# Kernel tuning notes

Hardware: AMD Instinct MI355X
Metric: run time of the kernel (lower is better)

The kernel has to match this reference:

```python
import jax, jax.numpy as jnp
import numpy as np
import math

B, T, C, E, H = 16, 256, 6, 512, 8


def setup_inputs() -> dict:
    key = jax.random.key(0)
    ks = jax.random.split(key, 5)
    std = 0.02
    return {
        "x": jax.random.normal(ks[0], (B, T, C, E), dtype=jnp.float32),
        "Wq": jax.random.normal(ks[1], (E, E), dtype=jnp.float32) * std,
        "bq": jnp.zeros((E,), dtype=jnp.float32),
        "Wk": jax.random.normal(ks[2], (E, E), dtype=jnp.float32) * std,
        "bk": jnp.zeros((E,), dtype=jnp.float32),
        "Wv": jax.random.normal(ks[3], (E, E), dtype=jnp.float32) * std,
        "bv": jnp.zeros((E,), dtype=jnp.float32),
        "Wp": jax.random.normal(ks[4], (E, E), dtype=jnp.float32) * std,
        "bp": jnp.zeros((E,), dtype=jnp.float32),
    }


def reference(x, Wq, bq, Wk, bk, Wv, bv, Wp, bp):
    b, t, c, e = x.shape
    hd = e // H
    # nn.Linear: y = x @ W^T + b, then view(B,T,C,H,hd).transpose(1,3) -> (B,H,C,T,hd)
    def heads(W, bias):
        y = jnp.einsum('btce,fe->btcf', x, W) + bias
        return y.reshape(b, t, c, H, hd).transpose(0, 3, 2, 1, 4)  # B,H,C,T,hd

    q = heads(Wq, bq)
    k = heads(Wk, bk)
    v = heads(Wv, bv)

    scale = 1.0 / math.sqrt(hd)
    att = jnp.einsum('bhctd,bhcsd->bhcts', q, k) * scale  # B,H,C,T,T
    causal = jnp.tril(jnp.ones((t, t), dtype=bool))
    att = jnp.where(causal, att, -jnp.inf)
    att = jax.nn.softmax(att, axis=-1)

    y = jnp.einsum('bhcts,bhcsd->bhctd', att, v)  # B,H,C,T,hd
    # permute(0,3,1,2,4) -> (B,T,H,C,hd), then view(B,T,C,E) (faithful to torch)
    y = y.transpose(0, 3, 1, 2, 4).reshape(b, t, c, e)
    return jnp.einsum('btce,fe->btcf', y, Wp) + bp
```

## Files before the change

### kernel.cpp

```cpp
#include <hip/hip_runtime.h>


typedef unsigned short u16;
typedef short bf16x8 __attribute__((ext_vector_type(8)));
typedef float f32x4 __attribute__((ext_vector_type(4)));
typedef u16 u16x4 __attribute__((ext_vector_type(4)));

#define MFMA16(a, b, c) __builtin_amdgcn_mfma_f32_16x16x32_bf16((a), (b), (c), 0, 0, 0)

__device__ __forceinline__ u16 f2b(float f) {
  union { float f; unsigned u; } v; v.f = f;
  unsigned r = v.u + 0x7fffu + ((v.u >> 16) & 1u);
  return (u16)(r >> 16);
}
__device__ __forceinline__ void gl_lds16(const void* g, void* l) {
  __builtin_amdgcn_global_load_lds(
      (const __attribute__((address_space(1))) void*)g,
      (__attribute__((address_space(3))) void*)l, 16, 0, 0);
}

__global__ void cvt_w(const float* W0, const float* W1, const float* W2,
                      const float* W3, u16* dst) {
  const float* src = (blockIdx.y == 0) ? W0 : (blockIdx.y == 1) ? W1
                   : (blockIdx.y == 2) ? W2 : W3;
  const int idx = (blockIdx.x * 256 + threadIdx.x) * 4;
  f32x4 v = *(const f32x4*)(src + idx);
  u16x4 o; o.x = f2b(v.x); o.y = f2b(v.y); o.z = f2b(v.z); o.w = f2b(v.w);
  *(u16x4*)(dst + (size_t)blockIdx.y * 262144 + idx) = o;
}

__global__ void cvt_x(const float* __restrict__ src, u16* __restrict__ dst) {
  const size_t idx = ((size_t)blockIdx.x * 256 + threadIdx.x) * 4;
  f32x4 v = *(const f32x4*)(src + idx);
  u16x4 o; o.x = f2b(v.x); o.y = f2b(v.y); o.z = f2b(v.z); o.w = f2b(v.w);
  *(u16x4*)(dst + idx) = o;
}

__global__ __launch_bounds__(256, 3) void gemm_bt(
    const u16* __restrict__ A,
    const u16* W0, const u16* W1, const u16* W2,
    const float* bs0, const float* bs1, const float* bs2,
    u16* O0, u16* O1, u16* O2,
    float* OF,
    int qkv_mode)
{
  const int z = blockIdx.z;
  const u16* W    = (z == 0) ? W0 : (z == 1) ? W1 : W2;
  const float* bs = (z == 0) ? bs0 : (z == 1) ? bs1 : bs2;
  u16* O          = (z == 0) ? O0 : (z == 1) ? O1 : O2;

  const int m0 = blockIdx.x * 128;
  const int n0 = blockIdx.y * 128;

  __shared__ u16 As[128 * 32];
  __shared__ u16 Bs[128 * 32];

  const int tid  = threadIdx.x;
  const int lane = tid & 63;
  const int wv   = tid >> 6;
  const int r    = lane & 15;
  const int qd   = lane >> 4;
  const int wm   = (wv & 1) * 64;
  const int wn   = (wv >> 1) * 64;

  f32x4 acc[4][4] = {};

  for (int k0 = 0; k0 < 512; k0 += 32) {
    __syncthreads();
    #pragma unroll
    for (int it = 0; it < 2; ++it) {
      const int flat = (it * 256 + tid) * 16;
      const int row  = flat >> 6;
      const int swc  = (flat >> 4) & 3;
      const int gc   = (swc - (row >> 1)) & 3;
      gl_lds16((const char*)A + (size_t)(m0 + row) * 1024 + k0 * 2 + gc * 16,
               (char*)As + flat);
      gl_lds16((const char*)W + (size_t)(n0 + row) * 1024 + k0 * 2 + gc * 16,
               (char*)Bs + flat);
    }
    __syncthreads();

    bf16x8 af[4], bf[4];
    #pragma unroll
    for (int mt = 0; mt < 4; ++mt) {
      const int row = wm + mt * 16 + r;
      const int sw  = (qd + (row >> 1)) & 3;
      af[mt] = *(const bf16x8*)((const char*)As + row * 64 + sw * 16);
    }
    #pragma unroll
    for (int nt = 0; nt < 4; ++nt) {
      const int row = wn + nt * 16 + r;
      const int sw  = (qd + (row >> 1)) & 3;
      bf[nt] = *(const bf16x8*)((const char*)Bs + row * 64 + sw * 16);
    }
    #pragma unroll
    for (int mt = 0; mt < 4; ++mt)
      #pragma unroll
      for (int nt = 0; nt < 4; ++nt)
        acc[mt][nt] = MFMA16(af[mt], bf[nt], acc[mt][nt]);
  }

  float bv[4];
  #pragma unroll
  for (int nt = 0; nt < 4; ++nt) bv[nt] = bs[n0 + wn + nt * 16 + r];

  if (qkv_mode) {
    #pragma unroll
    for (int mt = 0; mt < 4; ++mt) {
      #pragma unroll
      for (int rr = 0; rr < 4; ++rr) {
        const int m   = m0 + wm + mt * 16 + qd * 4 + rr;
        const int b   = m / 1536;
        const int rem = m - b * 1536;
        const int t   = rem / 6;
        const int c   = rem - t * 6;
        #pragma unroll
        for (int nt = 0; nt < 4; ++nt) {
          const int f = n0 + wn + nt * 16 + r;
          const int h = f >> 6;
          const int d = f & 63;
          const size_t addr = ((((size_t)b * 8 + h) * 6 + c) * 256 + t) * 64 + d;
          O[addr] = f2b(acc[mt][nt][rr] + bv[nt]);
        }
      }
    }
  } else {
    #pragma unroll
    for (int mt = 0; mt < 4; ++mt) {
      #pragma unroll
      for (int rr = 0; rr < 4; ++rr) {
        const int m = m0 + wm + mt * 16 + qd * 4 + rr;
        #pragma unroll
        for (int nt = 0; nt < 4; ++nt) {
          const int f = n0 + wn + nt * 16 + r;
          OF[(size_t)m * 512 + f] = acc[mt][nt][rr] + bv[nt];
        }
      }
    }
  }
}

__global__ __launch_bounds__(512, 2) void attn(
    const u16* __restrict__ q_ws, const u16* __restrict__ k_ws,
    const u16* __restrict__ v_ws, u16* __restrict__ y_ws)
{
  const int blk = blockIdx.x;
  const int b   = blk / 48;
  const int h   = (blk / 6) % 8;
  const int c   = blk % 6;
  const size_t base = (size_t)blk * 256 * 64;

  __shared__ u16 Ks[128 * 72];
  __shared__ u16 Vts[64 * 136];
  __shared__ u16 Ps[8][16 * 72];

  const int tid  = threadIdx.x;
  const int lane = tid & 63;
  const int wv   = tid >> 6;
  const int r    = lane & 15;
  const int qd   = lane >> 4;

  const int tiles[2] = { wv, 15 - wv };

  bf16x8 qf[2][2];
  #pragma unroll
  for (int ti = 0; ti < 2; ++ti)
    #pragma unroll
    for (int kc = 0; kc < 2; ++kc)
      qf[ti][kc] = *(const bf16x8*)(q_ws + base +
                     (size_t)(tiles[ti] * 16 + r) * 64 + kc * 32 + qd * 8);

  f32x4 o_acc[2][4] = {};
  float l_acc[2][4] = {{0.f,0.f,0.f,0.f},{0.f,0.f,0.f,0.f}};

  for (int sc = 0; sc < 2; ++sc) {
    __syncthreads();
    #pragma unroll
    for (int it = 0; it < 2; ++it) {
      const int idx = it * 512 + tid;
      const int row = idx >> 3;
      const int c8  = idx & 7;
      *(bf16x8*)(Ks + row * 72 + c8 * 8) =
          *(const bf16x8*)(k_ws + base + (size_t)(sc * 128 + row) * 64 + c8 * 8);
    }
    {
      const int jl = tid & 127;
      const int d0 = (tid >> 7) * 16;
      #pragma unroll
      for (int dd = 0; dd < 16; dd += 8) {
        bf16x8 vv = *(const bf16x8*)(v_ws + base +
                       (size_t)(sc * 128 + jl) * 64 + d0 + dd);
        #pragma unroll
        for (int e = 0; e < 8; ++e)
          Vts[(d0 + dd + e) * 136 + jl] = ((u16*)&vv)[e];
      }
    }
    __syncthreads();

    #pragma unroll
    for (int ti = 0; ti < 2; ++ti) {
      const int mt  = tiles[ti];
      const int i0  = mt * 16;
      const int nch = (mt >> 2) + 1;
      #pragma unroll
      for (int jcl = 0; jcl < 2; ++jcl) {
        const int jc = sc * 2 + jcl;
        if (jc >= nch) continue;
        const int j0l = jcl * 64;
        const int j0g = sc * 128 + j0l;

        f32x4 s[4] = {};
        #pragma unroll
        for (int nt = 0; nt < 4; ++nt)
          #pragma unroll
          for (int kc = 0; kc < 2; ++kc) {
            bf16x8 kf = *(const bf16x8*)(Ks + (j0l + nt * 16 + r) * 72 +
                                         kc * 32 + qd * 8);
            s[nt] = MFMA16(qf[ti][kc], kf, s[nt]);
          }

        #pragma unroll
        for (int nt = 0; nt < 4; ++nt)
          #pragma unroll
          for (int rr = 0; rr < 4; ++rr) {
            const int i = i0 + qd * 4 + rr;
            const int j = j0g + nt * 16 + r;
            float p = __builtin_exp2f(fminf(s[nt][rr], 500.f) *
                                      0.1803368801111244f);
            if (j > i) p = 0.f;
            l_acc[ti][rr] += p;
            Ps[wv][(qd * 4 + rr) * 72 + nt * 16 + r] = f2b(p);
          }
        asm volatile("s_waitcnt lgkmcnt(0)" ::: "memory");

        bf16x8 pf[2];
        #pragma unroll
        for (int kc = 0; kc < 2; ++kc)
          pf[kc] = *(const bf16x8*)(Ps[wv] + r * 72 + kc * 32 + qd * 8);
        #pragma unroll
        for (int ntd = 0; ntd < 4; ++ntd)
          #pragma unroll
          for (int kc = 0; kc < 2; ++kc) {
            bf16x8 vf = *(const bf16x8*)(Vts + (ntd * 16 + r) * 136 +
                                         j0l + kc * 32 + qd * 8);
            o_acc[ti][ntd] = MFMA16(pf[kc], vf, o_acc[ti][ntd]);
          }
      }
    }
  }

  const size_t obase = ((size_t)b * 256) * 3072 + h * 384 + c * 64;
  #pragma unroll
  for (int ti = 0; ti < 2; ++ti) {
    const int i0 = tiles[ti] * 16;
    float linv[4];
    #pragma unroll
    for (int rr = 0; rr < 4; ++rr) {
      float sum = l_acc[ti][rr];
      sum += __shfl_xor(sum, 1, 16);
      sum += __shfl_xor(sum, 2, 16);
      sum += __shfl_xor(sum, 4, 16);
      sum += __shfl_xor(sum, 8, 16);
      linv[rr] = 1.f / sum;
    }
    #pragma unroll
    for (int ntd = 0; ntd < 4; ++ntd)
      #pragma unroll
      for (int rr = 0; rr < 4; ++rr) {
        const int t = i0 + qd * 4 + rr;
        const int d = ntd * 16 + r;
        y_ws[obase + (size_t)t * 3072 + d] = f2b(o_acc[ti][ntd][rr] * linv[rr]);
      }
  }
}

extern "C" void kernel_launch(void* const* d_in, const int* in_sizes, int n_in,
                              void* d_out, int out_size, void* d_ws, size_t ws_size,
                              hipStream_t stream) {
  const float* x  = (const float*)d_in[0];
  const float* Wq = (const float*)d_in[1];
  const float* bq = (const float*)d_in[2];
  const float* Wk = (const float*)d_in[3];
  const float* bk = (const float*)d_in[4];
  const float* Wv = (const float*)d_in[5];
  const float* bv = (const float*)d_in[6];
  const float* Wp = (const float*)d_in[7];
  const float* bp = (const float*)d_in[8];
  float* out = (float*)d_out;

  const size_t PER_B = 256 * 6 * 512;
  const size_t WSEG  = 4 * 262144;

  int NB = 16;
  while (NB > 1 && (WSEG + (size_t)5 * NB * PER_B) * 2 > ws_size) NB >>= 1;

  u16* wbf = (u16*)d_ws;
  u16* Wqb = wbf;
  u16* Wkb = wbf + 262144;
  u16* Wvb = wbf + 2 * 262144;
  u16* Wpb = wbf + 3 * 262144;

  const size_t slab = (size_t)NB * PER_B;
  u16* xbf  = wbf + WSEG;
  u16* q_ws = xbf + slab;
  u16* k_ws = q_ws + slab;
  u16* v_ws = k_ws + slab;
  u16* y_ws = v_ws + slab;

  cvt_w<<<dim3(256, 4), 256, 0, stream>>>(Wq, Wk, Wv, Wp, wbf);

  const int nslab = 16 / NB;
  for (int s = 0; s < nslab; ++s) {
    const float* x_s  = x   + (size_t)s * NB * PER_B;
    float*      out_s = out + (size_t)s * NB * PER_B;
    cvt_x<<<dim3(NB * 768), 256, 0, stream>>>(x_s, xbf);
    gemm_bt<<<dim3(NB * 12, 4, 3), 256, 0, stream>>>(
        xbf, Wqb, Wkb, Wvb, bq, bk, bv, q_ws, k_ws, v_ws, nullptr, 1);
    attn<<<dim3(NB * 48), 512, 0, stream>>>(q_ws, k_ws, v_ws, y_ws);
    gemm_bt<<<dim3(NB * 12, 4, 1), 256, 0, stream>>>(
        y_ws, Wpb, Wpb, Wpb, bp, bp, bp, nullptr, nullptr, nullptr, out_s, 0);
  }
}
```

Baseline: 222.4 us.

## Rewrite projection GEMM with 256x128 tiles and triple-buffered async LDS pipeline

Replaces the 128x128, K=32 single-buffered GEMM with a 512-thread 256x128 tile kernel using K=64 stages in a three-deep LDS ring. Global-to-LDS loads for stage k+2 are issued while stage k is computed, with explicit vmcnt waits, and MFMA sections run at raised wave priority. The LDS layout switches to an XOR swizzle. This aims to hide global load latency and cut barrier overhead per FLOP, at the cost of much more LDS per block (about 144KB), which limits occupancy, and fewer blocks per launch.

```diff
diff --git a/kernel.cpp b/kernel.cpp
--- a/kernel.cpp
+++ b/kernel.cpp
@@ -36,7 +36,7 @@
   *(u16x4*)(dst + idx) = o;
 }
 
-__global__ __launch_bounds__(256, 3) void gemm_bt(
+__global__ __launch_bounds__(512, 2) void gemm256(
     const u16* __restrict__ A,
     const u16* W0, const u16* W1, const u16* W2,
     const float* bs0, const float* bs1, const float* bs2,
@@ -49,74 +49,125 @@
   const float* bs = (z == 0) ? bs0 : (z == 1) ? bs1 : bs2;
   u16* O          = (z == 0) ? O0 : (z == 1) ? O1 : O2;
 
-  const int m0 = blockIdx.x * 128;
+  const int m0 = blockIdx.x * 256;
   const int n0 = blockIdx.y * 128;
 
-  __shared__ u16 As[128 * 32];
-  __shared__ u16 Bs[128 * 32];
+  __shared__ u16 As[3][256 * 64];
+  __shared__ u16 Bs[3][128 * 64];
 
   const int tid  = threadIdx.x;
   const int lane = tid & 63;
   const int wv   = tid >> 6;
   const int r    = lane & 15;
   const int qd   = lane >> 4;
-  const int wm   = (wv & 1) * 64;
-  const int wn   = (wv >> 1) * 64;
+  const int wr   = wv >> 1;
+  const int wc   = wv & 1;
+
+  const char* srcA[4]; const char* srcB[2];
+  int flatA[4], flatB[2];
+  #pragma unroll
+  for (int j = 0; j < 4; ++j) {
+    const int flat = (j * 512 + tid) * 16;
+    const int row  = flat >> 7;
+    const int c16  = (flat >> 4) & 7;
+    flatA[j] = flat;
+    srcA[j]  = (const char*)A + (size_t)(m0 + row) * 1024 + ((c16 ^ (row & 7)) << 4);
+  }
+  #pragma unroll
+  for (int j = 0; j < 2; ++j) {
+    const int flat = (j * 512 + tid) * 16;
+    const int row  = flat >> 7;
+    const int c16  = (flat >> 4) & 7;
+    flatB[j] = flat;
+    srcB[j]  = (const char*)W + (size_t)(n0 + row) * 1024 + ((c16 ^ (row & 7)) << 4);
+  }
+
+  const int sw   = (r & 7) << 4;
+  const int colq = qd * 16;
+  int arow[4], brow[4];
+  #pragma unroll
+  for (int mt = 0; mt < 4; ++mt) arow[mt] = (wr * 64 + mt * 16 + r) * 128;
+  #pragma unroll
+  for (int nt = 0; nt < 4; ++nt) brow[nt] = (wc * 64 + nt * 16 + r) * 128;
 
   f32x4 acc[4][4] = {};
 
-  for (int k0 = 0; k0 < 512; k0 += 32) {
-    __syncthreads();
-    #pragma unroll
-    for (int it = 0; it < 2; ++it) {
-      const int flat = (it * 256 + tid) * 16;
-      const int row  = flat >> 6;
-      const int swc  = (flat >> 4) & 3;
-      const int gc   = (swc - (row >> 1)) & 3;
-      gl_lds16((const char*)A + (size_t)(m0 + row) * 1024 + k0 * 2 + gc * 16,
-               (char*)As + flat);
-      gl_lds16((const char*)W + (size_t)(n0 + row) * 1024 + k0 * 2 + gc * 16,
-               (char*)Bs + flat);
-    }
-    __syncthreads();
-
-    bf16x8 af[4], bf[4];
+  #pragma unroll
+  for (int tt = 0; tt < 2; ++tt) {
+    #pragma unroll
+    for (int j = 0; j < 4; ++j)
+      gl_lds16(srcA[j] + tt * 128, (char*)As[tt] + flatA[j]);
+    #pragma unroll
+    for (int j = 0; j < 2; ++j)
+      gl_lds16(srcB[j] + tt * 128, (char*)Bs[tt] + flatB[j]);
+  }
+  asm volatile("s_waitcnt vmcnt(6)\n\ts_barrier" ::: "memory");
+
+  #pragma unroll
+  for (int kt = 0; kt < 8; ++kt) {
+    const int cb  = kt % 3;
+    const int pb  = (kt + 2) % 3;
+    const bool pre = (kt + 2) < 8;
+
+    #pragma unroll
+    for (int kc = 0; kc < 2; ++kc) {
+      const int co = (kc * 64 + colq);
+      bf16x8 af[4], bf[4];
+      #pragma unroll
+      for (int mt = 0; mt < 4; ++mt)
+        af[mt] = *(const bf16x8*)((const char*)As[cb] + arow[mt] + (co ^ sw));
+      #pragma unroll
+      for (int nt = 0; nt < 4; ++nt)
+        bf[nt] = *(const bf16x8*)((const char*)Bs[cb] + brow[nt] + (co ^ sw));
+
+      if (pre) {
+        if (kc == 0) {
+          gl_lds16(srcA[0] + (kt + 2) * 128, (char*)As[pb] + flatA[0]);
+          gl_lds16(srcA[1] + (kt + 2) * 128, (char*)As[pb] + flatA[1]);
+          gl_lds16(srcB[0] + (kt + 2) * 128, (char*)Bs[pb] + flatB[0]);
+        } else {
+          gl_lds16(srcA[2] + (kt + 2) * 128, (char*)As[pb] + flatA[2]);
+          gl_lds16(srcA[3] + (kt + 2) * 128, (char*)As[pb] + flatA[3]);
+          gl_lds16(srcB[1] + (kt + 2) * 128, (char*)Bs[pb] + flatB[1]);
+        }
+      }
+
+      asm volatile("s_barrier" ::: "memory");
+      __builtin_amdgcn_s_setprio(1);
+      #pragma unroll
+      for (int mt = 0; mt < 4; ++mt)
+        #pragma unroll
+        for (int nt = 0; nt < 4; ++nt)
+          acc[mt][nt] = MFMA16(af[mt], bf[nt], acc[mt][nt]);
+      __builtin_amdgcn_s_setprio(0);
+
+      if (kc == 0) {
+        asm volatile("s_barrier" ::: "memory");
+      } else if (kt < 6) {
+        asm volatile("s_waitcnt vmcnt(6)\n\ts_barrier" ::: "memory");
+      } else if (kt == 6) {
+        asm volatile("s_waitcnt vmcnt(0)\n\ts_barrier" ::: "memory");
+      }
+    }
+  }
+
+  float bv[4];
+  #pragma unroll
+  for (int nt = 0; nt < 4; ++nt) bv[nt] = bs[n0 + wc * 64 + nt * 16 + r];
+
+  if (qkv_mode) {
     #pragma unroll
     for (int mt = 0; mt < 4; ++mt) {
-      const int row = wm + mt * 16 + r;
-      const int sw  = (qd + (row >> 1)) & 3;
-      af[mt] = *(const bf16x8*)((const char*)As + row * 64 + sw * 16);
-    }
-    #pragma unroll
-    for (int nt = 0; nt < 4; ++nt) {
-      const int row = wn + nt * 16 + r;
-      const int sw  = (qd + (row >> 1)) & 3;
-      bf[nt] = *(const bf16x8*)((const char*)Bs + row * 64 + sw * 16);
-    }
-    #pragma unroll
-    for (int mt = 0; mt < 4; ++mt)
-      #pragma unroll
-      for (int nt = 0; nt < 4; ++nt)
-        acc[mt][nt] = MFMA16(af[mt], bf[nt], acc[mt][nt]);
-  }
-
-  float bv[4];
-  #pragma unroll
-  for (int nt = 0; nt < 4; ++nt) bv[nt] = bs[n0 + wn + nt * 16 + r];
-
-  if (qkv_mode) {
-    #pragma unroll
-    for (int mt = 0; mt < 4; ++mt) {
       #pragma unroll
       for (int rr = 0; rr < 4; ++rr) {
-        const int m   = m0 + wm + mt * 16 + qd * 4 + rr;
+        const int m   = m0 + wr * 64 + mt * 16 + qd * 4 + rr;
         const int b   = m / 1536;
         const int rem = m - b * 1536;
         const int t   = rem / 6;
         const int c   = rem - t * 6;
         #pragma unroll
         for (int nt = 0; nt < 4; ++nt) {
-          const int f = n0 + wn + nt * 16 + r;
+          const int f = n0 + wc * 64 + nt * 16 + r;
           const int h = f >> 6;
           const int d = f & 63;
           const size_t addr = ((((size_t)b * 8 + h) * 6 + c) * 256 + t) * 64 + d;
@@ -129,10 +180,10 @@
     for (int mt = 0; mt < 4; ++mt) {
       #pragma unroll
       for (int rr = 0; rr < 4; ++rr) {
-        const int m = m0 + wm + mt * 16 + qd * 4 + rr;
+        const int m = m0 + wr * 64 + mt * 16 + qd * 4 + rr;
         #pragma unroll
         for (int nt = 0; nt < 4; ++nt) {
-          const int f = n0 + wn + nt * 16 + r;
+          const int f = n0 + wc * 64 + nt * 16 + r;
           OF[(size_t)m * 512 + f] = acc[mt][nt][rr] + bv[nt];
         }
       }
@@ -314,10 +365,10 @@
     const float* x_s  = x   + (size_t)s * NB * PER_B;
     float*      out_s = out + (size_t)s * NB * PER_B;
     cvt_x<<<dim3(NB * 768), 256, 0, stream>>>(x_s, xbf);
-    gemm_bt<<<dim3(NB * 12, 4, 3), 256, 0, stream>>>(
+    gemm256<<<dim3(NB * 6, 4, 3), 512, 0, stream>>>(
         xbf, Wqb, Wkb, Wvb, bq, bk, bv, q_ws, k_ws, v_ws, nullptr, 1);
     attn<<<dim3(NB * 48), 512, 0, stream>>>(q_ws, k_ws, v_ws, y_ws);
-    gemm_bt<<<dim3(NB * 12, 4, 1), 256, 0, stream>>>(
+    gemm256<<<dim3(NB * 6, 4, 1), 512, 0, stream>>>(
         y_ws, Wpb, Wpb, Wpb, bp, bp, bp, nullptr, nullptr, nullptr, out_s, 0);
   }
 }
```

Result: slower. 233.7 us (+5.1%).

## Triple-buffer GEMM K-loop with async LDS loads and reorder grid for A reuse

Applied to the files above, without the earlier changes.

The projection GEMM now keeps three LDS stages and prefetches K-tiles two steps ahead using global_load_lds, with one waitcnt plus barrier per iteration in place of two syncthreads around each load. The grid is remapped so that the blocks sharing an A row tile (all N tiles and all Q/K/V weights) are adjacent in blockIdx.x, which should improve L2 reuse of activations. LDS use grows threefold (48KB per block), which may limit occupancy against the launch bound of 3.

```diff
diff --git a/kernel.cpp b/kernel.cpp
--- a/kernel.cpp
+++ b/kernel.cpp
@@ -44,16 +44,17 @@
     float* OF,
     int qkv_mode)
 {
-  const int z = blockIdx.z;
-  const u16* W    = (z == 0) ? W0 : (z == 1) ? W1 : W2;
-  const float* bs = (z == 0) ? bs0 : (z == 1) ? bs1 : bs2;
-  u16* O          = (z == 0) ? O0 : (z == 1) ? O1 : O2;
-
-  const int m0 = blockIdx.x * 128;
-  const int n0 = blockIdx.y * 128;
-
-  __shared__ u16 As[128 * 32];
-  __shared__ u16 Bs[128 * 32];
+  const int bx  = blockIdx.x;
+  const int sel = bx >> 2;
+  const u16* W    = (sel == 0) ? W0 : (sel == 1) ? W1 : W2;
+  const float* bs = (sel == 0) ? bs0 : (sel == 1) ? bs1 : bs2;
+  u16* O          = (sel == 0) ? O0 : (sel == 1) ? O1 : O2;
+
+  const int m0 = blockIdx.y * 128;
+  const int nl = (bx & 3) * 128;
+
+  __shared__ u16 As[3][128 * 32];
+  __shared__ u16 Bs[3][128 * 32];
 
   const int tid  = threadIdx.x;
   const int lane = tid & 63;
@@ -63,46 +64,70 @@
   const int wm   = (wv & 1) * 64;
   const int wn   = (wv >> 1) * 64;
 
+  const char* gA[2]; const char* gB[2]; int fl[2];
+  #pragma unroll
+  for (int it = 0; it < 2; ++it) {
+    const int flat = (it * 256 + tid) * 16;
+    const int row  = flat >> 6;
+    const int gc   = (((flat >> 4) & 3) - (row >> 1)) & 3;
+    fl[it] = flat;
+    gA[it] = (const char*)A + (size_t)(m0 + row) * 1024 + gc * 16;
+    gB[it] = (const char*)W + (size_t)(nl + row) * 1024 + gc * 16;
+  }
+
   f32x4 acc[4][4] = {};
 
-  for (int k0 = 0; k0 < 512; k0 += 32) {
-    __syncthreads();
+  #pragma unroll
+  for (int tt = 0; tt < 2; ++tt)
     #pragma unroll
     for (int it = 0; it < 2; ++it) {
-      const int flat = (it * 256 + tid) * 16;
-      const int row  = flat >> 6;
-      const int swc  = (flat >> 4) & 3;
-      const int gc   = (swc - (row >> 1)) & 3;
-      gl_lds16((const char*)A + (size_t)(m0 + row) * 1024 + k0 * 2 + gc * 16,
-               (char*)As + flat);
-      gl_lds16((const char*)W + (size_t)(n0 + row) * 1024 + k0 * 2 + gc * 16,
-               (char*)Bs + flat);
-    }
-    __syncthreads();
+      gl_lds16(gA[it] + tt * 64, (char*)As[tt] + fl[it]);
+      gl_lds16(gB[it] + tt * 64, (char*)Bs[tt] + fl[it]);
+    }
+  asm volatile("s_waitcnt vmcnt(4)\n\ts_barrier" ::: "memory");
+
+  #pragma unroll
+  for (int kt = 0; kt < 16; ++kt) {
+    const int cb = kt % 3;
+    const int pb = (kt + 2) % 3;
+
+    if (kt + 2 < 16) {
+      #pragma unroll
+      for (int it = 0; it < 2; ++it) {
+        gl_lds16(gA[it] + (kt + 2) * 64, (char*)As[pb] + fl[it]);
+        gl_lds16(gB[it] + (kt + 2) * 64, (char*)Bs[pb] + fl[it]);
+      }
+    }
 
     bf16x8 af[4], bf[4];
     #pragma unroll
     for (int mt = 0; mt < 4; ++mt) {
       const int row = wm + mt * 16 + r;
       const int sw  = (qd + (row >> 1)) & 3;
-      af[mt] = *(const bf16x8*)((const char*)As + row * 64 + sw * 16);
+      af[mt] = *(const bf16x8*)((const char*)As[cb] + row * 64 + sw * 16);
     }
     #pragma unroll
     for (int nt = 0; nt < 4; ++nt) {
       const int row = wn + nt * 16 + r;
       const int sw  = (qd + (row >> 1)) & 3;
-      bf[nt] = *(const bf16x8*)((const char*)Bs + row * 64 + sw * 16);
+      bf[nt] = *(const bf16x8*)((const char*)Bs[cb] + row * 64 + sw * 16);
     }
     #pragma unroll
     for (int mt = 0; mt < 4; ++mt)
       #pragma unroll
       for (int nt = 0; nt < 4; ++nt)
         acc[mt][nt] = MFMA16(af[mt], bf[nt], acc[mt][nt]);
+
+    if (kt < 14) {
+      asm volatile("s_waitcnt vmcnt(4)\n\ts_barrier" ::: "memory");
+    } else if (kt == 14) {
+      asm volatile("s_waitcnt vmcnt(0)\n\ts_barrier" ::: "memory");
+    }
   }
 
   float bv[4];
   #pragma unroll
-  for (int nt = 0; nt < 4; ++nt) bv[nt] = bs[n0 + wn + nt * 16 + r];
+  for (int nt = 0; nt < 4; ++nt) bv[nt] = bs[nl + wn + nt * 16 + r];
 
   if (qkv_mode) {
     #pragma unroll
@@ -116,7 +141,7 @@
         const int c   = rem - t * 6;
         #pragma unroll
         for (int nt = 0; nt < 4; ++nt) {
-          const int f = n0 + wn + nt * 16 + r;
+          const int f = nl + wn + nt * 16 + r;
           const int h = f >> 6;
           const int d = f & 63;
           const size_t addr = ((((size_t)b * 8 + h) * 6 + c) * 256 + t) * 64 + d;
@@ -132,7 +157,7 @@
         const int m = m0 + wm + mt * 16 + qd * 4 + rr;
         #pragma unroll
         for (int nt = 0; nt < 4; ++nt) {
-          const int f = n0 + wn + nt * 16 + r;
+          const int f = nl + wn + nt * 16 + r;
           OF[(size_t)m * 512 + f] = acc[mt][nt][rr] + bv[nt];
         }
       }
@@ -314,10 +339,10 @@
     const float* x_s  = x   + (size_t)s * NB * PER_B;
     float*      out_s = out + (size_t)s * NB * PER_B;
     cvt_x<<<dim3(NB * 768), 256, 0, stream>>>(x_s, xbf);
-    gemm_bt<<<dim3(NB * 12, 4, 3), 256, 0, stream>>>(
+    gemm_bt<<<dim3(12, NB * 12, 1), 256, 0, stream>>>(
         xbf, Wqb, Wkb, Wvb, bq, bk, bv, q_ws, k_ws, v_ws, nullptr, 1);
     attn<<<dim3(NB * 48), 512, 0, stream>>>(q_ws, k_ws, v_ws, y_ws);
-    gemm_bt<<<dim3(NB * 12, 4, 1), 256, 0, stream>>>(
+    gemm_bt<<<dim3(4, NB * 12, 1), 256, 0, stream>>>(
         y_ws, Wpb, Wpb, Wpb, bp, bp, bp, nullptr, nullptr, nullptr, out_s, 0);
   }
 }
```

After: 225.1 us. About the same (+1.2%).

## Replace GEMM with 256x256 double-buffered 8-wave pipelined MFMA kernel

Applied to the files above, without the earlier changes.

Replaces the 128x128, 256-thread GEMM with a 256x256-tile, 512-thread kernel. It uses a K-step of 64, double-buffered LDS staged by global_load_lds, an XOR swizzle, and interleaved load/MFMA phases with s_setprio and explicit vmcnt waits. The Q/K/V weights are treated as one contiguous 1536-row matrix indexed by blockIdx.y instead of a z dimension. This is meant to hide global load latency and raise arithmetic intensity per block. The cost is much larger LDS use (128 KB), higher register pressure and fewer blocks per grid (96 for the projection), which may underfill the GPU.

```diff
diff --git a/kernel.cpp b/kernel.cpp
--- a/kernel.cpp
+++ b/kernel.cpp
@@ -36,105 +36,157 @@
   *(u16x4*)(dst + idx) = o;
 }
 
-__global__ __launch_bounds__(256, 3) void gemm_bt(
-    const u16* __restrict__ A,
-    const u16* W0, const u16* W1, const u16* W2,
-    const float* bs0, const float* bs1, const float* bs2,
-    u16* O0, u16* O1, u16* O2,
-    float* OF,
-    int qkv_mode)
+#define BARX() __builtin_amdgcn_s_barrier()
+#define WLGK() asm volatile("s_waitcnt lgkmcnt(0)" ::: "memory")
+#define VMW(n) asm volatile("s_waitcnt vmcnt(" #n ")" ::: "memory")
+
+#define STG_A(buf, half, t) do { \
+  gl_lds16(aS0 + (size_t)(half) * 131072 + (t) * 128,         ldsA##buf + (half) * 16384 + fo0); \
+  gl_lds16(aS0 + (size_t)(half) * 131072 + 65536 + (t) * 128, ldsA##buf + (half) * 16384 + fo1); \
+} while (0)
+#define STG_B(buf, half, t) do { \
+  gl_lds16(bS0 + (size_t)(half) * 131072 + (t) * 128,         ldsB##buf + (half) * 16384 + fo0); \
+  gl_lds16(bS0 + (size_t)(half) * 131072 + 65536 + (t) * 128, ldsB##buf + (half) * 16384 + fo1); \
+} while (0)
+
+#define LDA(buf, qm) \
+  _Pragma("unroll") for (int mtq = 0; mtq < 4; ++mtq) { \
+    const int row_ = wr128 + (qm) * 64 + mtq * 16 + r; \
+    af[mtq][0] = *(const bf16x8*)(ldsA##buf + row_ * 128 + lo0); \
+    af[mtq][1] = *(const bf16x8*)(ldsA##buf + row_ * 128 + lo1); \
+  }
+#define LDB(buf, qn) \
+  _Pragma("unroll") for (int ntq = 0; ntq < 2; ++ntq) { \
+    const int row_ = wc64 + (qn) * 32 + ntq * 16 + r; \
+    bf[ntq][0] = *(const bf16x8*)(ldsB##buf + row_ * 128 + lo0); \
+    bf[ntq][1] = *(const bf16x8*)(ldsB##buf + row_ * 128 + lo1); \
+  }
+
+#define MM(qm, qn) \
+  _Pragma("unroll") for (int mtq = 0; mtq < 4; ++mtq) \
+    _Pragma("unroll") for (int ntq = 0; ntq < 2; ++ntq) { \
+      acc[(qm)*4+mtq][(qn)*2+ntq] = MFMA16(af[mtq][0], bf[ntq][0], acc[(qm)*4+mtq][(qn)*2+ntq]); \
+      acc[(qm)*4+mtq][(qn)*2+ntq] = MFMA16(af[mtq][1], bf[ntq][1], acc[(qm)*4+mtq][(qn)*2+ntq]); \
+    }
+
+#define MFMA_PHASE(qm, qn) do { \
+  BARX(); WLGK(); \
+  __builtin_amdgcn_s_setprio(1); \
+  MM(qm, qn); \
+  __builtin_amdgcn_s_setprio(0); \
+} while (0)
+
+__global__ __launch_bounds__(512, 2) void gemm8(
+    const u16* __restrict__ A, const u16* __restrict__ Wf,
+    const float* b0, const float* b1, const float* b2,
+    u16* O0, u16* O1, u16* O2, float* OF, int qkv_mode)
 {
-  const int z = blockIdx.z;
-  const u16* W    = (z == 0) ? W0 : (z == 1) ? W1 : W2;
-  const float* bs = (z == 0) ? bs0 : (z == 1) ? bs1 : bs2;
-  u16* O          = (z == 0) ? O0 : (z == 1) ? O1 : O2;
-
-  const int m0 = blockIdx.x * 128;
-  const int n0 = blockIdx.y * 128;
-
-  __shared__ u16 As[128 * 32];
-  __shared__ u16 Bs[128 * 32];
-
-  const int tid  = threadIdx.x;
-  const int lane = tid & 63;
-  const int wv   = tid >> 6;
-  const int r    = lane & 15;
-  const int qd   = lane >> 4;
-  const int wm   = (wv & 1) * 64;
-  const int wn   = (wv >> 1) * 64;
-
-  f32x4 acc[4][4] = {};
-
-  for (int k0 = 0; k0 < 512; k0 += 32) {
-    __syncthreads();
-    #pragma unroll
-    for (int it = 0; it < 2; ++it) {
-      const int flat = (it * 256 + tid) * 16;
-      const int row  = flat >> 6;
-      const int swc  = (flat >> 4) & 3;
-      const int gc   = (swc - (row >> 1)) & 3;
-      gl_lds16((const char*)A + (size_t)(m0 + row) * 1024 + k0 * 2 + gc * 16,
-               (char*)As + flat);
-      gl_lds16((const char*)W + (size_t)(n0 + row) * 1024 + k0 * 2 + gc * 16,
-               (char*)Bs + flat);
-    }
-    __syncthreads();
-
-    bf16x8 af[4], bf[4];
-    #pragma unroll
-    for (int mt = 0; mt < 4; ++mt) {
-      const int row = wm + mt * 16 + r;
-      const int sw  = (qd + (row >> 1)) & 3;
-      af[mt] = *(const bf16x8*)((const char*)As + row * 64 + sw * 16);
-    }
-    #pragma unroll
-    for (int nt = 0; nt < 4; ++nt) {
-      const int row = wn + nt * 16 + r;
-      const int sw  = (qd + (row >> 1)) & 3;
-      bf[nt] = *(const bf16x8*)((const char*)Bs + row * 64 + sw * 16);
-    }
-    #pragma unroll
-    for (int mt = 0; mt < 4; ++mt)
-      #pragma unroll
-      for (int nt = 0; nt < 4; ++nt)
-        acc[mt][nt] = MFMA16(af[mt], bf[nt], acc[mt][nt]);
-  }
-
-  float bv[4];
+  const int m0   = blockIdx.x * 256;
+  const int by   = blockIdx.y;
+  const int n0   = by * 256;
+  const int sel  = by >> 1;
+  const int ncol = (by & 1) * 256;
+
+  __shared__ u16 As[2][256 * 64];
+  __shared__ u16 Bs[2][256 * 64];
+
+  char* ldsA0 = (char*)&As[0][0];  char* ldsA1 = (char*)&As[1][0];
+  char* ldsB0 = (char*)&Bs[0][0];  char* ldsB1 = (char*)&Bs[1][0];
+
+  const int tid   = threadIdx.x;
+  const int lane  = tid & 63;
+  const int wv    = tid >> 6;
+  const int r     = lane & 15;
+  const int qd    = lane >> 4;
+  const int wr128 = (wv >> 2) * 128;
+  const int wc64  = (wv & 3) * 64;
+
+  const int fo0  = tid * 16;
+  const int fo1  = 8192 + tid * 16;
+  const int cswz = ((tid & 7) ^ ((tid >> 3) & 7)) << 4;
+  const char* aS0 = (const char*)A  + (size_t)(m0 + (tid >> 3)) * 1024 + cswz;
+  const char* bS0 = (const char*)Wf + (size_t)(n0 + (tid >> 3)) * 1024 + cswz;
+
+  const int lo0 = ( qd      ^ (r & 7)) << 4;
+  const int lo1 = ((4 + qd) ^ (r & 7)) << 4;
+
+  f32x4  acc[8][4] = {};
+  bf16x8 af[4][2], bf[2][2];
+
+  STG_B(0, 0, 0); STG_B(0, 1, 0); STG_A(0, 0, 0); STG_A(0, 1, 0);
+  STG_B(1, 0, 1); STG_B(1, 1, 1); STG_A(1, 0, 1); STG_A(1, 1, 1);
+  VMW(8); BARX();
+
   #pragma unroll
-  for (int nt = 0; nt < 4; ++nt) bv[nt] = bs[n0 + wn + nt * 16 + r];
+  for (int i = 0; i < 4; ++i) {
+    const int v = 2 * i + 1;
+    const int w = 2 * i + 2;
+    const int x2 = 2 * i + 3;
+
+    LDA(0, 0) LDB(0, 0)  STG_B(1, 1, v);
+    MFMA_PHASE(0, 0);  BARX();
+
+    LDA(0, 1)            STG_A(1, 0, v);
+    MFMA_PHASE(1, 0);  BARX();
+
+    LDB(0, 1)            STG_A(1, 1, v);
+    MFMA_PHASE(1, 1);  BARX();
+
+    LDA(0, 0)            if (i < 3) { STG_B(0, 0, w); }
+    MFMA_PHASE(0, 1);
+    if (i < 3) { VMW(2); } else { VMW(0); }
+    BARX();
+
+    LDA(1, 0) LDB(1, 0)  if (i < 3) { STG_B(0, 1, w); }
+    MFMA_PHASE(0, 0);  BARX();
+
+    LDA(1, 1)            if (i < 3) { STG_A(0, 0, w); }
+    MFMA_PHASE(1, 0);  BARX();
+
+    LDB(1, 1)            if (i < 3) { STG_A(0, 1, w); }
+    MFMA_PHASE(1, 1);  BARX();
+
+    LDA(1, 0)            if (i < 3) { STG_B(1, 0, x2); }
+    MFMA_PHASE(0, 1);
+    if (i < 3) { VMW(2); }
+    BARX();
+  }
+
+  float bvv[4];
+  const float* bp_ = (sel == 0) ? b0 : (sel == 1) ? b1 : b2;
+  #pragma unroll
+  for (int nt = 0; nt < 4; ++nt) bvv[nt] = bp_[ncol + wc64 + nt * 16 + r];
 
   if (qkv_mode) {
-    #pragma unroll
-    for (int mt = 0; mt < 4; ++mt) {
+    u16* O = (sel == 0) ? O0 : (sel == 1) ? O1 : O2;
+    #pragma unroll
+    for (int mt = 0; mt < 8; ++mt) {
       #pragma unroll
       for (int rr = 0; rr < 4; ++rr) {
-        const int m   = m0 + wm + mt * 16 + qd * 4 + rr;
+        const int m   = m0 + wr128 + mt * 16 + qd * 4 + rr;
         const int b   = m / 1536;
         const int rem = m - b * 1536;
         const int t   = rem / 6;
         const int c   = rem - t * 6;
         #pragma unroll
         for (int nt = 0; nt < 4; ++nt) {
-          const int f = n0 + wn + nt * 16 + r;
-          const int h = f >> 6;
-          const int d = f & 63;
+          const int colm = ncol + wc64 + nt * 16 + r;
+          const int h = colm >> 6;
+          const int d = colm & 63;
           const size_t addr = ((((size_t)b * 8 + h) * 6 + c) * 256 + t) * 64 + d;
-          O[addr] = f2b(acc[mt][nt][rr] + bv[nt]);
+          O[addr] = f2b(acc[mt][nt][rr] + bvv[nt]);
         }
       }
     }
   } else {
     #pragma unroll
-    for (int mt = 0; mt < 4; ++mt) {
+    for (int mt = 0; mt < 8; ++mt) {
       #pragma unroll
       for (int rr = 0; rr < 4; ++rr) {
-        const int m = m0 + wm + mt * 16 + qd * 4 + rr;
-        #pragma unroll
-        for (int nt = 0; nt < 4; ++nt) {
-          const int f = n0 + wn + nt * 16 + r;
-          OF[(size_t)m * 512 + f] = acc[mt][nt][rr] + bv[nt];
-        }
+        const int m = m0 + wr128 + mt * 16 + qd * 4 + rr;
+        #pragma unroll
+        for (int nt = 0; nt < 4; ++nt)
+          OF[(size_t)m * 512 + ncol + wc64 + nt * 16 + r] = acc[mt][nt][rr] + bvv[nt];
       }
     }
   }
@@ -296,8 +348,6 @@
 
   u16* wbf = (u16*)d_ws;
   u16* Wqb = wbf;
-  u16* Wkb = wbf + 262144;
-  u16* Wvb = wbf + 2 * 262144;
   u16* Wpb = wbf + 3 * 262144;
 
   const size_t slab = (size_t)NB * PER_B;
@@ -314,10 +364,10 @@
     const float* x_s  = x   + (size_t)s * NB * PER_B;
     float*      out_s = out + (size_t)s * NB * PER_B;
     cvt_x<<<dim3(NB * 768), 256, 0, stream>>>(x_s, xbf);
-    gemm_bt<<<dim3(NB * 12, 4, 3), 256, 0, stream>>>(
-        xbf, Wqb, Wkb, Wvb, bq, bk, bv, q_ws, k_ws, v_ws, nullptr, 1);
+    gemm8<<<dim3(NB * 6, 6), 512, 0, stream>>>(
+        xbf, Wqb, bq, bk, bv, q_ws, k_ws, v_ws, nullptr, 1);
     attn<<<dim3(NB * 48), 512, 0, stream>>>(q_ws, k_ws, v_ws, y_ws);
-    gemm_bt<<<dim3(NB * 12, 4, 1), 256, 0, stream>>>(
-        y_ws, Wpb, Wpb, Wpb, bp, bp, bp, nullptr, nullptr, nullptr, out_s, 0);
-  }
-}
+    gemm8<<<dim3(NB * 6, 2), 512, 0, stream>>>(
+        y_ws, Wpb, bp, bp, bp, nullptr, nullptr, nullptr, out_s, 0);
+  }
+}
```

Result: slower. 229.5 us (+3.2%).
